# Optimization experiments

Hardware: AMD Instinct MI355X
Metric: run time of the kernel (lower is better)

Reference implementation:

```python
import jax, jax.numpy as jnp
import numpy as np

N = 50000   # nodes
R = 50      # relations
B = 30      # bases
F_IN = 64   # input features
H = 64      # hidden channels
C = 8       # classes
E = 1000000 # edges


def setup_inputs() -> dict:
    key = jax.random.key(0)
    ks = jax.random.split(key, 16)
    x = jax.random.normal(ks[0], (N, F_IN), jnp.float32)
    edge_index = jax.random.randint(ks[1], (2, E), 0, N)
    edge_type = jax.random.randint(ks[2], (E,), 0, R)
    inp = {"x": x, "edge_index": edge_index, "edge_type": edge_type}
    dims = [(F_IN, H), (H, H), (H, C)]
    i = 3
    for l, (din, dout) in enumerate(dims):
        s = 1.0 / np.sqrt(din)
        inp[f"bases{l}"] = jax.random.normal(ks[i], (B, din, dout), jnp.float32) * s; i += 1
        inp[f"comp{l}"] = jax.random.normal(ks[i], (R, B), jnp.float32) / np.sqrt(B); i += 1
        inp[f"root{l}"] = jax.random.normal(ks[i], (din, dout), jnp.float32) * s; i += 1
        inp[f"bias{l}"] = jnp.zeros((dout,), jnp.float32); i += 1
    return inp


def _rgcn(x, bases, comp, root, bias, src, seg):
    # Per-relation mean aggregation (PyG RGCNConv default aggr='mean'):
    # segment id = dst * R + relation. Mean of source features per (dst, rel),
    # then basis-decomposed transform (linearity lets transform follow the mean).
    din = x.shape[1]
    sums = jax.ops.segment_sum(x[src], seg, num_segments=N * R)          # [N*R, din]
    cnt = jax.ops.segment_sum(jnp.ones((seg.shape[0],), x.dtype), seg, num_segments=N * R)
    inv = jnp.where(cnt > 0, 1.0 / jnp.maximum(cnt, 1.0), 0.0)
    agg = (sums * inv[:, None]).reshape(N, R, din)                        # [N, R, din]
    t = jnp.einsum('nri,rb->nbi', agg, comp)                              # [N, B, din]
    msg = jnp.einsum('nbi,bio->no', t, bases)                             # [N, dout]
    return msg + x @ root + bias


def reference(x, edge_index, edge_type,
              bases0, comp0, root0, bias0,
              bases1, comp1, root1, bias1,
              bases2, comp2, root2, bias2):
    src, dst = edge_index[0], edge_index[1]
    seg = dst * R + edge_type
    params = [(bases0, comp0, root0, bias0),
              (bases1, comp1, root1, bias1),
              (bases2, comp2, root2, bias2)]
    x1 = x
    for b, c, r, bi in params:
        x1 = _rgcn(x, b, c, r, bi, src, seg)
        x = jax.nn.relu(x1)
    # original returns log_softmax of the last conv's pre-ReLU output
    return jax.nn.log_softmax(x1, axis=1)
```

## Files before the change

kernel.cpp:

```cpp
#include <hip/hip_runtime.h>
#include <hip/hip_bf16.h>
#include <stdint.h>

#define NN   50000
#define RR   50
#define BB   30
#define DIN  64
#define EE   1000000
#define KTOT (BB*DIN + DIN)
#define NBW  16
#define ROWE (KTOT + 8)
#define CPAD 32

typedef __attribute__((ext_vector_type(8))) short short8;
typedef __attribute__((ext_vector_type(4))) float floatx4;

#define RFL(x) __builtin_amdgcn_readfirstlane(x)


__global__ void k_hist(const int* __restrict__ dst, const int* __restrict__ et,
                       int* __restrict__ cnt, int* __restrict__ dcount) {
    int e = blockIdx.x * 256 + threadIdx.x;
    if (e < EE) {
        int d = dst[e], r = et[e];
        atomicAdd(&cnt[d * RR + r], 1);
        atomicAdd(&dcount[d], 1);
    }
}

__global__ void k_scan1(const int* __restrict__ dcount, int* __restrict__ doff,
                        int* __restrict__ bsum) {
    __shared__ int sh[256];
    int t = threadIdx.x;
    int i = blockIdx.x * 256 + t;
    int v = (i < NN) ? dcount[i] : 0;
    sh[t] = v;
    __syncthreads();
    for (int s = 1; s < 256; s <<= 1) {
        int add = (t >= s) ? sh[t - s] : 0;
        __syncthreads();
        sh[t] += add;
        __syncthreads();
    }
    int incl = sh[t];
    if (i < NN) doff[i] = incl - v;
    if (t == 255) bsum[blockIdx.x] = incl;
}

__global__ void k_scan2(int* __restrict__ bsum, int nbv) {
    __shared__ int sh[256];
    int t = threadIdx.x;
    int v = (t < nbv) ? bsum[t] : 0;
    sh[t] = v;
    __syncthreads();
    for (int s = 1; s < 256; s <<= 1) {
        int add = (t >= s) ? sh[t - s] : 0;
        __syncthreads();
        sh[t] += add;
        __syncthreads();
    }
    if (t < nbv) bsum[t] = sh[t] - v;
}

__global__ void k_scan3(int* __restrict__ doff, const int* __restrict__ bsum) {
    int i = blockIdx.x * 256 + threadIdx.x;
    if (i < NN) doff[i] += bsum[blockIdx.x];
}

__global__ void k_scatter(const int* __restrict__ src, const int* __restrict__ dst,
                          const int* __restrict__ et, const int* __restrict__ cnt,
                          const int* __restrict__ doff, int* __restrict__ cursor,
                          int4* __restrict__ epack) {
    int e = blockIdx.x * 256 + threadIdx.x;
    if (e < EE) {
        int d = dst[e], r = et[e], s = src[e];
        int p = doff[d] + atomicAdd(&cursor[d], 1);
        float a = 1.0f / (float)cnt[d * RR + r];
        epack[p] = make_int4(s, r, __float_as_int(a), 0);
    }
}

__global__ void k_cast_x(const float* __restrict__ x, __hip_bfloat16* __restrict__ h) {
    int i = blockIdx.x * 256 + threadIdx.x;
    if (i < NN * DIN) h[i] = __float2bfloat16(x[i]);
}

__global__ void k_prep_comp3(const float* __restrict__ c0, const float* __restrict__ c1,
                             const float* __restrict__ c2, float* __restrict__ cp) {
    int idx = blockIdx.x * 256 + threadIdx.x;
    if (idx < 3 * RR * CPAD) {
        int l = idx / (RR * CPAD);
        int rem = idx - l * (RR * CPAD);
        int r = rem / CPAD, i = rem - r * CPAD;
        const float* c = (l == 0) ? c0 : (l == 1) ? c1 : c2;
        cp[idx] = (i < BB) ? c[r * BB + i] : 0.f;
    }
}

__global__ void k_prep_w3(const float* __restrict__ b0, const float* __restrict__ r0,
                          const float* __restrict__ b1, const float* __restrict__ r1,
                          const float* __restrict__ b2, const float* __restrict__ r2,
                          short* __restrict__ wt) {
    int idx = blockIdx.x * 256 + threadIdx.x;
    if (idx >= 144 * KTOT) return;
    int row = idx / KTOT, k = idx - row * KTOT;
    const float* bs; const float* rt; int o, dout;
    if (row < 64)       { bs = b0; rt = r0; o = row;        dout = 64; }
    else if (row < 128) { bs = b1; rt = r1; o = row - 64;   dout = 64; }
    else                { bs = b2; rt = r2; o = row - 128;  dout = 8;  }
    float v = 0.f;
    if (o < dout)
        v = (k < BB * DIN) ? bs[k * dout + o] : rt[(k - BB * DIN) * dout + o];
    __hip_bfloat16 hb = __float2bfloat16(v);
    wt[idx] = *reinterpret_cast<const short*>(&hb);
}

template <int DOUT, bool RELU>
__global__ __launch_bounds__(1024, 8)
void k_fused(const __hip_bfloat16* __restrict__ xin,
             const int4* __restrict__ epack,
             const int* __restrict__ doff, const int* __restrict__ dcount,
             const float* __restrict__ compP,
             const short* __restrict__ Wt,
             const float* __restrict__ bias,
             void* __restrict__ outp) {
    __shared__ __align__(16) char smem_raw[NBW * ROWE * 2];
    auto t_tile = reinterpret_cast<__hip_bfloat16(*)[ROWE]>(smem_raw);
    const int tid  = threadIdx.x;
    const int lane = tid & 63;
    const int wv   = RFL(tid >> 6);
    const int node0 = blockIdx.x * NBW;

    {
        const int j = wv;
        const int n = node0 + j;
        floatx4 acc[8];
#pragma unroll
        for (int u = 0; u < 8; ++u) acc[u] = (floatx4){0.f, 0.f, 0.f, 0.f};
        const int beg = RFL(doff[n]), cnt = RFL(dcount[n]);
        const int nch = cnt >> 2;

        if (nch > 0) {
            int4 cr0 = epack[beg + 0], cr1 = epack[beg + 1];
            int4 cr2 = epack[beg + 2], cr3 = epack[beg + 3];
            float g0 = __bfloat162float(xin[RFL(cr0.x) * DIN + lane]);
            float g1 = __bfloat162float(xin[RFL(cr1.x) * DIN + lane]);
            float g2 = __bfloat162float(xin[RFL(cr2.x) * DIN + lane]);
            float g3 = __bfloat162float(xin[RFL(cr3.x) * DIN + lane]);
            const int b1 = beg + ((1 < nch) ? 4 : 0);
            int4 nr0 = epack[b1 + 0], nr1 = epack[b1 + 1];
            int4 nr2 = epack[b1 + 2], nr3 = epack[b1 + 3];

            for (int c = 0; c < nch; ++c) {
                const int cc = (c + 2 < nch) ? (c + 2) : (nch - 1);
                const int bp = beg + 4 * cc;
                int4 p0 = epack[bp + 0], p1 = epack[bp + 1];
                int4 p2 = epack[bp + 2], p3 = epack[bp + 3];
                float h0 = __bfloat162float(xin[RFL(nr0.x) * DIN + lane]);
                float h1 = __bfloat162float(xin[RFL(nr1.x) * DIN + lane]);
                float h2 = __bfloat162float(xin[RFL(nr2.x) * DIN + lane]);
                float h3 = __bfloat162float(xin[RFL(nr3.x) * DIN + lane]);
                {
                    const float a0 = __int_as_float(RFL(cr0.z));
                    const floatx4* q0 = (const floatx4*)(compP + RFL(cr0.y) * CPAD);
                    const float xv0 = g0 * a0;
                    const floatx4 w0 = {xv0, xv0, xv0, xv0};
#pragma unroll
                    for (int u = 0; u < 8; ++u) acc[u] = q0[u] * w0 + acc[u];
                    const float a1 = __int_as_float(RFL(cr1.z));
                    const floatx4* q1 = (const floatx4*)(compP + RFL(cr1.y) * CPAD);
                    const float xv1 = g1 * a1;
                    const floatx4 w1 = {xv1, xv1, xv1, xv1};
#pragma unroll
                    for (int u = 0; u < 8; ++u) acc[u] = q1[u] * w1 + acc[u];
                    const float a2 = __int_as_float(RFL(cr2.z));
                    const floatx4* q2 = (const floatx4*)(compP + RFL(cr2.y) * CPAD);
                    const float xv2 = g2 * a2;
                    const floatx4 w2 = {xv2, xv2, xv2, xv2};
#pragma unroll
                    for (int u = 0; u < 8; ++u) acc[u] = q2[u] * w2 + acc[u];
                    const float a3 = __int_as_float(RFL(cr3.z));
                    const floatx4* q3 = (const floatx4*)(compP + RFL(cr3.y) * CPAD);
                    const float xv3 = g3 * a3;
                    const floatx4 w3 = {xv3, xv3, xv3, xv3};
#pragma unroll
                    for (int u = 0; u < 8; ++u) acc[u] = q3[u] * w3 + acc[u];
                }
                cr0 = nr0; cr1 = nr1; cr2 = nr2; cr3 = nr3;
                nr0 = p0;  nr1 = p1;  nr2 = p2;  nr3 = p3;
                g0 = h0; g1 = h1; g2 = h2; g3 = h3;
            }
        }
        for (int e = nch * 4; e < cnt; ++e) {
            int4 ep = epack[beg + e];
            const int s = RFL(ep.x), r = RFL(ep.y);
            const float a = __int_as_float(RFL(ep.z));
            const float xv = __bfloat162float(xin[s * DIN + lane]) * a;
            const floatx4* c = (const floatx4*)(compP + r * CPAD);
            const floatx4 w = {xv, xv, xv, xv};
#pragma unroll
            for (int u = 0; u < 8; ++u) acc[u] = c[u] * w + acc[u];
        }
        const float xself = __bfloat162float(xin[n * DIN + lane]);
#pragma unroll
        for (int b = 0; b < BB; ++b)
            t_tile[j][b * DIN + lane] = __float2bfloat16(acc[b >> 2][b & 3]);
        t_tile[j][BB * DIN + lane] = __float2bfloat16(xself);
    }
    __syncthreads();

    const int m = lane & 15;
    const int q = lane >> 4;
    int kk0, nsteps, col_base, kpart;
    if (DOUT == 64) {
        kpart = wv >> 2;
        col_base = (wv & 3) * 16;
        kk0    = (kpart <= 1) ? kpart * 16 : (kpart == 2 ? 32 : 47);
        nsteps = (kpart <= 1) ? 16 : 15;
    } else {
        kpart = wv;
        col_base = 0;
        kk0    = (kpart < 14) ? kpart * 4 : (kpart == 14 ? 56 : 59);
        nsteps = (kpart < 14) ? 4 : 3;
    }
    const __hip_bfloat16* arow = &t_tile[m][q * 8];
    const short* brow = Wt + (size_t)(col_base + m) * KTOT + q * 8;

    floatx4 acc0 = {0.f, 0.f, 0.f, 0.f};
    floatx4 acc1 = {0.f, 0.f, 0.f, 0.f};
    int s = 0;
    for (; s + 2 <= nsteps; s += 2) {
        const int kk = kk0 + s;
        short8 a0 = *reinterpret_cast<const short8*>(arow + kk * 32);
        short8 b0 = *reinterpret_cast<const short8*>(brow + kk * 32);
        short8 a1 = *reinterpret_cast<const short8*>(arow + (kk + 1) * 32);
        short8 b1 = *reinterpret_cast<const short8*>(brow + (kk + 1) * 32);
        acc0 = __builtin_amdgcn_mfma_f32_16x16x32_bf16(a0, b0, acc0, 0, 0, 0);
        acc1 = __builtin_amdgcn_mfma_f32_16x16x32_bf16(a1, b1, acc1, 0, 0, 0);
    }
    if (s < nsteps) {
        const int kk = kk0 + s;
        short8 a0 = *reinterpret_cast<const short8*>(arow + kk * 32);
        short8 b0 = *reinterpret_cast<const short8*>(brow + kk * 32);
        acc0 = __builtin_amdgcn_mfma_f32_16x16x32_bf16(a0, b0, acc0, 0, 0, 0);
    }
    floatx4 P = acc0 + acc1;

    __syncthreads();
    float* red = (float*)smem_raw;

    if (DOUT == 64) {
        if (kpart > 0) {
            const int slot = (wv & 3) * 3 + (kpart - 1);
            const int off = (slot * 64 + lane) * 6;
            red[off] = P[0]; red[off + 1] = P[1]; red[off + 2] = P[2]; red[off + 3] = P[3];
        }
        __syncthreads();
        if (kpart == 0) {
#pragma unroll
            for (int t = 0; t < 3; ++t) {
                const int off = (((wv & 3) * 3 + t) * 64 + lane) * 6;
                P[0] += red[off]; P[1] += red[off + 1];
                P[2] += red[off + 2]; P[3] += red[off + 3];
            }
            const int o = col_base + m;
            const float bi = bias[o];
#pragma unroll
            for (int r = 0; r < 4; ++r) {
                const int n = node0 + q * 4 + r;
                float v = P[r] + bi;
                if (RELU) {
                    v = fmaxf(v, 0.f);
                    reinterpret_cast<__hip_bfloat16*>(outp)[(size_t)n * DOUT + o] =
                        __float2bfloat16(v);
                } else {
                    reinterpret_cast<float*>(outp)[(size_t)n * DOUT + o] = v;
                }
            }
        }
    } else {
        if (kpart > 0) {
            const int off = ((kpart - 1) * 64 + lane) * 6;
            red[off] = P[0]; red[off + 1] = P[1]; red[off + 2] = P[2]; red[off + 3] = P[3];
        }
        __syncthreads();
        if (kpart == 0) {
#pragma unroll
            for (int w = 0; w < 15; ++w) {
                const int off = (w * 64 + lane) * 6;
                P[0] += red[off]; P[1] += red[off + 1];
                P[2] += red[off + 2]; P[3] += red[off + 3];
            }
            if (m < DOUT) {
                const int o = m;
                const float bi = bias[o];
#pragma unroll
                for (int r = 0; r < 4; ++r) {
                    const int n = node0 + q * 4 + r;
                    reinterpret_cast<float*>(outp)[(size_t)n * DOUT + o] = P[r] + bi;
                }
            }
        }
    }
}

__global__ void k_lsm(const float* __restrict__ pre, float* __restrict__ out) {
    int n = blockIdx.x * 256 + threadIdx.x;
    if (n < NN) {
        float v[8];
        float mx = -1e30f;
#pragma unroll
        for (int c = 0; c < 8; ++c) { v[c] = pre[n * 8 + c]; mx = fmaxf(mx, v[c]); }
        float s = 0.f;
#pragma unroll
        for (int c = 0; c < 8; ++c) s += expf(v[c] - mx);
        float ls = logf(s);
#pragma unroll
        for (int c = 0; c < 8; ++c) out[n * 8 + c] = v[c] - mx - ls;
    }
}

extern "C" void kernel_launch(void* const* d_in, const int* in_sizes, int n_in,
                              void* d_out, int out_size, void* d_ws, size_t ws_size,
                              hipStream_t stream) {
    const float* x     = (const float*)d_in[0];
    const int*   eidx  = (const int*)d_in[1];
    const int*   etype = (const int*)d_in[2];
    const float* bases0 = (const float*)d_in[3];
    const float* comp0  = (const float*)d_in[4];
    const float* root0  = (const float*)d_in[5];
    const float* bias0  = (const float*)d_in[6];
    const float* bases1 = (const float*)d_in[7];
    const float* comp1  = (const float*)d_in[8];
    const float* root1  = (const float*)d_in[9];
    const float* bias1  = (const float*)d_in[10];
    const float* bases2 = (const float*)d_in[11];
    const float* comp2  = (const float*)d_in[12];
    const float* root2  = (const float*)d_in[13];
    const float* bias2  = (const float*)d_in[14];
    const int* srcp = eidx;
    const int* dstp = eidx + EE;

    char* p = (char*)d_ws;
    auto carve = [&](size_t bytes) -> char* {
        char* r = p;
        p += (bytes + 255) & ~(size_t)255;
        return r;
    };
    int*  cnt    = (int*)carve((size_t)NN * RR * sizeof(int));
    int*  dcount = (int*)carve((size_t)NN * sizeof(int));
    int*  cursor = (int*)carve((size_t)NN * sizeof(int));
    int*  doff   = (int*)carve((size_t)NN * sizeof(int));
    int*  bsum   = (int*)carve(256 * sizeof(int));
    int4* epack  = (int4*)carve((size_t)EE * sizeof(int4));
    __hip_bfloat16* h0 = (__hip_bfloat16*)carve((size_t)NN * DIN * 2);
    __hip_bfloat16* h1 = (__hip_bfloat16*)carve((size_t)NN * DIN * 2);
    __hip_bfloat16* h2 = (__hip_bfloat16*)carve((size_t)NN * DIN * 2);
    float* pre = (float*)carve((size_t)NN * 8 * sizeof(float));
    short* wtA = (short*)carve((size_t)144 * KTOT * sizeof(short));
    float* cpA = (float*)carve((size_t)3 * RR * CPAD * sizeof(float));

    hipMemsetAsync(cnt, 0, (size_t)NN * (RR + 2) * sizeof(int) + 512, stream);

    const int EB = (EE + 255) / 256;
    const int NB = (NN + 255) / 256;
    k_hist<<<EB, 256, 0, stream>>>(dstp, etype, cnt, dcount);
    k_scan1<<<NB, 256, 0, stream>>>(dcount, doff, bsum);
    k_scan2<<<1, 256, 0, stream>>>(bsum, NB);
    k_scan3<<<NB, 256, 0, stream>>>(doff, bsum);
    k_scatter<<<EB, 256, 0, stream>>>(srcp, dstp, etype, cnt, doff, cursor, epack);
    k_cast_x<<<(NN * DIN + 255) / 256, 256, 0, stream>>>(x, h0);
    k_prep_comp3<<<(3 * RR * CPAD + 255) / 256, 256, 0, stream>>>(comp0, comp1, comp2, cpA);
    k_prep_w3<<<(144 * KTOT + 255) / 256, 256, 0, stream>>>(bases0, root0, bases1, root1,
                                                            bases2, root2, wtA);

    short* wt0 = wtA;
    short* wt1 = wtA + (size_t)64 * KTOT;
    short* wt2 = wtA + (size_t)128 * KTOT;
    float* cp0 = cpA;
    float* cp1 = cpA + RR * CPAD;
    float* cp2 = cpA + 2 * RR * CPAD;

    const int NF = NN / NBW;
    k_fused<64, true ><<<NF, 1024, 0, stream>>>(h0, epack, doff, dcount, cp0, wt0, bias0, (void*)h1);
    k_fused<64, true ><<<NF, 1024, 0, stream>>>(h1, epack, doff, dcount, cp1, wt1, bias1, (void*)h2);
    k_fused<8,  false><<<NF, 1024, 0, stream>>>(h2, epack, doff, dcount, cp2, wt2, bias2, (void*)pre);
    k_lsm<<<NB, 256, 0, stream>>>(pre, (float*)d_out);
}
```

Before: 598.5 us.

## Process two nodes per wave with packed 8-byte edge records and 512-thread blocks

The fused RGCN kernel now uses 512-thread blocks, and each wave aggregates two destination nodes in one software-pipelined loop. Partial 4-edge chunks are padded with zeroed records, which removes the scalar tail loop. Edge records shrink from int4 to int2 by packing source and relation into one word, halving edge-stream traffic. The per-destination degree atomic is dropped and degrees are recomputed in the scan from the per-relation counts. The GEMM K-split is rebalanced for 8 waves. The packing assumes node ids below 65536 and uses fewer waves per block, which may reduce latency hiding.

```diff
diff --git a/kernel.cpp b/kernel.cpp
--- a/kernel.cpp
+++ b/kernel.cpp
@@ -19,21 +19,26 @@
 
 
 __global__ void k_hist(const int* __restrict__ dst, const int* __restrict__ et,
-                       int* __restrict__ cnt, int* __restrict__ dcount) {
+                       int* __restrict__ cnt) {
     int e = blockIdx.x * 256 + threadIdx.x;
     if (e < EE) {
         int d = dst[e], r = et[e];
         atomicAdd(&cnt[d * RR + r], 1);
-        atomicAdd(&dcount[d], 1);
-    }
-}
-
-__global__ void k_scan1(const int* __restrict__ dcount, int* __restrict__ doff,
-                        int* __restrict__ bsum) {
+    }
+}
+
+__global__ void k_scan1(const int* __restrict__ cnt, int* __restrict__ dcount,
+                        int* __restrict__ doff, int* __restrict__ bsum) {
     __shared__ int sh[256];
     int t = threadIdx.x;
     int i = blockIdx.x * 256 + t;
-    int v = (i < NN) ? dcount[i] : 0;
+    int v = 0;
+    if (i < NN) {
+        const int* c = cnt + (size_t)i * RR;
+#pragma unroll
+        for (int r = 0; r < RR; ++r) v += c[r];
+        dcount[i] = v;
+    }
     sh[t] = v;
     __syncthreads();
     for (int s = 1; s < 256; s <<= 1) {
@@ -70,13 +75,13 @@
 __global__ void k_scatter(const int* __restrict__ src, const int* __restrict__ dst,
                           const int* __restrict__ et, const int* __restrict__ cnt,
                           const int* __restrict__ doff, int* __restrict__ cursor,
-                          int4* __restrict__ epack) {
+                          int2* __restrict__ ep2) {
     int e = blockIdx.x * 256 + threadIdx.x;
     if (e < EE) {
         int d = dst[e], r = et[e], s = src[e];
         int p = doff[d] + atomicAdd(&cursor[d], 1);
         float a = 1.0f / (float)cnt[d * RR + r];
-        epack[p] = make_int4(s, r, __float_as_int(a), 0);
+        ep2[p] = make_int2(s | (r << 16), __float_as_int(a));
     }
 }
 
@@ -115,10 +120,37 @@
     wt[idx] = *reinterpret_cast<const short*>(&hb);
 }
 
+
+#define LOADREC(u, q0, q1, q2, q3) do {                                         \
+    const int _u  = (u);                                                        \
+    const int _b  = (_u < nchA) ? (begA + 4*_u) : (begB + 4*(_u - nchA));       \
+    const int _rm = (_u < nchA) ? (cntA - 4*_u) : (cntB - 4*(_u - nchA));       \
+    q0 = ep2[_b];     q1 = ep2[_b + 1];                                         \
+    q2 = ep2[_b + 2]; q3 = ep2[_b + 3];                                         \
+    q1.x = (_rm > 1) ? q1.x : 0;  q1.y = (_rm > 1) ? q1.y : 0;                  \
+    q2.x = (_rm > 2) ? q2.x : 0;  q2.y = (_rm > 2) ? q2.y : 0;                  \
+    q3.x = (_rm > 3) ? q3.x : 0;  q3.y = (_rm > 3) ? q3.y : 0;                  \
+} while (0)
+
+#define GATH(q) ((unsigned)xin16[(RFL((q).x) & 0xFFFF) * DIN + lane])
+
+#define EDGE_FMA(q, g, ACC) do {                                                \
+    const int   _sx = RFL((q).x);                                               \
+    const float _a  = __int_as_float(RFL((q).y));                               \
+    const floatx4* _c = (const floatx4*)(compP + (_sx >> 16) * CPAD);           \
+    const float _g  = __uint_as_float((g) << 16);              \
+    const float _xv = _g * _a;                                                  \
+    const floatx4 _w = {_xv, _xv, _xv, _xv};                                    \
+    ACC[0] = _c[0] * _w + ACC[0];  ACC[1] = _c[1] * _w + ACC[1];                \
+    ACC[2] = _c[2] * _w + ACC[2];  ACC[3] = _c[3] * _w + ACC[3];                \
+    ACC[4] = _c[4] * _w + ACC[4];  ACC[5] = _c[5] * _w + ACC[5];                \
+    ACC[6] = _c[6] * _w + ACC[6];  ACC[7] = _c[7] * _w + ACC[7];                \
+} while (0)
+
 template <int DOUT, bool RELU>
-__global__ __launch_bounds__(1024, 8)
+__global__ __launch_bounds__(512, 4)
 void k_fused(const __hip_bfloat16* __restrict__ xin,
-             const int4* __restrict__ epack,
+             const int2* __restrict__ ep2,
              const int* __restrict__ doff, const int* __restrict__ dcount,
              const float* __restrict__ compP,
              const short* __restrict__ Wt,
@@ -126,86 +158,63 @@
              void* __restrict__ outp) {
     __shared__ __align__(16) char smem_raw[NBW * ROWE * 2];
     auto t_tile = reinterpret_cast<__hip_bfloat16(*)[ROWE]>(smem_raw);
+    const unsigned short* xin16 = reinterpret_cast<const unsigned short*>(xin);
     const int tid  = threadIdx.x;
     const int lane = tid & 63;
     const int wv   = RFL(tid >> 6);
     const int node0 = blockIdx.x * NBW;
+    const int nA = node0 + wv;
+    const int nB = node0 + wv + 8;
 
     {
-        const int j = wv;
-        const int n = node0 + j;
-        floatx4 acc[8];
-#pragma unroll
-        for (int u = 0; u < 8; ++u) acc[u] = (floatx4){0.f, 0.f, 0.f, 0.f};
-        const int beg = RFL(doff[n]), cnt = RFL(dcount[n]);
-        const int nch = cnt >> 2;
-
-        if (nch > 0) {
-            int4 cr0 = epack[beg + 0], cr1 = epack[beg + 1];
-            int4 cr2 = epack[beg + 2], cr3 = epack[beg + 3];
-            float g0 = __bfloat162float(xin[RFL(cr0.x) * DIN + lane]);
-            float g1 = __bfloat162float(xin[RFL(cr1.x) * DIN + lane]);
-            float g2 = __bfloat162float(xin[RFL(cr2.x) * DIN + lane]);
-            float g3 = __bfloat162float(xin[RFL(cr3.x) * DIN + lane]);
-            const int b1 = beg + ((1 < nch) ? 4 : 0);
-            int4 nr0 = epack[b1 + 0], nr1 = epack[b1 + 1];
-            int4 nr2 = epack[b1 + 2], nr3 = epack[b1 + 3];
-
-            for (int c = 0; c < nch; ++c) {
-                const int cc = (c + 2 < nch) ? (c + 2) : (nch - 1);
-                const int bp = beg + 4 * cc;
-                int4 p0 = epack[bp + 0], p1 = epack[bp + 1];
-                int4 p2 = epack[bp + 2], p3 = epack[bp + 3];
-                float h0 = __bfloat162float(xin[RFL(nr0.x) * DIN + lane]);
-                float h1 = __bfloat162float(xin[RFL(nr1.x) * DIN + lane]);
-                float h2 = __bfloat162float(xin[RFL(nr2.x) * DIN + lane]);
-                float h3 = __bfloat162float(xin[RFL(nr3.x) * DIN + lane]);
-                {
-                    const float a0 = __int_as_float(RFL(cr0.z));
-                    const floatx4* q0 = (const floatx4*)(compP + RFL(cr0.y) * CPAD);
-                    const float xv0 = g0 * a0;
-                    const floatx4 w0 = {xv0, xv0, xv0, xv0};
-#pragma unroll
-                    for (int u = 0; u < 8; ++u) acc[u] = q0[u] * w0 + acc[u];
-                    const float a1 = __int_as_float(RFL(cr1.z));
-                    const floatx4* q1 = (const floatx4*)(compP + RFL(cr1.y) * CPAD);
-                    const float xv1 = g1 * a1;
-                    const floatx4 w1 = {xv1, xv1, xv1, xv1};
-#pragma unroll
-                    for (int u = 0; u < 8; ++u) acc[u] = q1[u] * w1 + acc[u];
-                    const float a2 = __int_as_float(RFL(cr2.z));
-                    const floatx4* q2 = (const floatx4*)(compP + RFL(cr2.y) * CPAD);
-                    const float xv2 = g2 * a2;
-                    const floatx4 w2 = {xv2, xv2, xv2, xv2};
-#pragma unroll
-                    for (int u = 0; u < 8; ++u) acc[u] = q2[u] * w2 + acc[u];
-                    const float a3 = __int_as_float(RFL(cr3.z));
-                    const floatx4* q3 = (const floatx4*)(compP + RFL(cr3.y) * CPAD);
-                    const float xv3 = g3 * a3;
-                    const floatx4 w3 = {xv3, xv3, xv3, xv3};
-#pragma unroll
-                    for (int u = 0; u < 8; ++u) acc[u] = q3[u] * w3 + acc[u];
+        floatx4 accA[8], accB[8];
+#pragma unroll
+        for (int u = 0; u < 8; ++u) {
+            accA[u] = (floatx4){0.f, 0.f, 0.f, 0.f};
+            accB[u] = (floatx4){0.f, 0.f, 0.f, 0.f};
+        }
+        const unsigned selfA = (unsigned)xin16[nA * DIN + lane];
+        const unsigned selfB = (unsigned)xin16[nB * DIN + lane];
+
+        const int begA = RFL(doff[nA]), cntA = RFL(dcount[nA]);
+        const int begB = RFL(doff[nB]), cntB = RFL(dcount[nB]);
+        const int nchA = (cntA + 3) >> 2;
+        const int nchB = (cntB + 3) >> 2;
+        const int T = nchA + nchB;
+
+        if (T > 0) {
+            int2 c0, c1, c2, c3, n0, n1, n2, n3;
+            LOADREC(0, c0, c1, c2, c3);
+            unsigned g0 = GATH(c0), g1 = GATH(c1), g2 = GATH(c2), g3 = GATH(c3);
+            { const int u1 = (1 < T) ? 1 : 0; LOADREC(u1, n0, n1, n2, n3); }
+
+            for (int t = 0; t < T; ++t) {
+                int2 p0, p1, p2, p3;
+                { const int u2 = (t + 2 < T) ? (t + 2) : (T - 1);
+                  LOADREC(u2, p0, p1, p2, p3); }
+                unsigned h0 = GATH(n0), h1 = GATH(n1), h2 = GATH(n2), h3 = GATH(n3);
+                if (t < nchA) {
+                    EDGE_FMA(c0, g0, accA); EDGE_FMA(c1, g1, accA);
+                    EDGE_FMA(c2, g2, accA); EDGE_FMA(c3, g3, accA);
+                } else {
+                    EDGE_FMA(c0, g0, accB); EDGE_FMA(c1, g1, accB);
+                    EDGE_FMA(c2, g2, accB); EDGE_FMA(c3, g3, accB);
                 }
-                cr0 = nr0; cr1 = nr1; cr2 = nr2; cr3 = nr3;
-                nr0 = p0;  nr1 = p1;  nr2 = p2;  nr3 = p3;
+                c0 = n0; c1 = n1; c2 = n2; c3 = n3;
+                n0 = p0; n1 = p1; n2 = p2; n3 = p3;
                 g0 = h0; g1 = h1; g2 = h2; g3 = h3;
             }
         }
-        for (int e = nch * 4; e < cnt; ++e) {
-            int4 ep = epack[beg + e];
-            const int s = RFL(ep.x), r = RFL(ep.y);
-            const float a = __int_as_float(RFL(ep.z));
-            const float xv = __bfloat162float(xin[s * DIN + lane]) * a;
-            const floatx4* c = (const floatx4*)(compP + r * CPAD);
-            const floatx4 w = {xv, xv, xv, xv};
-#pragma unroll
-            for (int u = 0; u < 8; ++u) acc[u] = c[u] * w + acc[u];
-        }
-        const float xself = __bfloat162float(xin[n * DIN + lane]);
 #pragma unroll
         for (int b = 0; b < BB; ++b)
-            t_tile[j][b * DIN + lane] = __float2bfloat16(acc[b >> 2][b & 3]);
-        t_tile[j][BB * DIN + lane] = __float2bfloat16(xself);
+            t_tile[wv][b * DIN + lane] = __float2bfloat16(accA[b >> 2][b & 3]);
+        t_tile[wv][BB * DIN + lane] =
+            __float2bfloat16(__uint_as_float(selfA << 16));
+#pragma unroll
+        for (int b = 0; b < BB; ++b)
+            t_tile[wv + 8][b * DIN + lane] = __float2bfloat16(accB[b >> 2][b & 3]);
+        t_tile[wv + 8][BB * DIN + lane] =
+            __float2bfloat16(__uint_as_float(selfB << 16));
     }
     __syncthreads();
 
@@ -215,13 +224,13 @@
     if (DOUT == 64) {
         kpart = wv >> 2;
         col_base = (wv & 3) * 16;
-        kk0    = (kpart <= 1) ? kpart * 16 : (kpart == 2 ? 32 : 47);
-        nsteps = (kpart <= 1) ? 16 : 15;
+        kk0    = kpart * 31;
+        nsteps = 31;
     } else {
         kpart = wv;
         col_base = 0;
-        kk0    = (kpart < 14) ? kpart * 4 : (kpart == 14 ? 56 : 59);
-        nsteps = (kpart < 14) ? 4 : 3;
+        kk0    = (kpart < 7) ? kpart * 8 : 55;
+        nsteps = (kpart < 6) ? 8 : 7;
     }
     const __hip_bfloat16* arow = &t_tile[m][q * 8];
     const short* brow = Wt + (size_t)(col_base + m) * KTOT + q * 8;
@@ -250,19 +259,15 @@
     float* red = (float*)smem_raw;
 
     if (DOUT == 64) {
-        if (kpart > 0) {
-            const int slot = (wv & 3) * 3 + (kpart - 1);
-            const int off = (slot * 64 + lane) * 6;
+        if (kpart == 1) {
+            const int off = ((wv & 3) * 64 + lane) * 6;
             red[off] = P[0]; red[off + 1] = P[1]; red[off + 2] = P[2]; red[off + 3] = P[3];
         }
         __syncthreads();
         if (kpart == 0) {
-#pragma unroll
-            for (int t = 0; t < 3; ++t) {
-                const int off = (((wv & 3) * 3 + t) * 64 + lane) * 6;
-                P[0] += red[off]; P[1] += red[off + 1];
-                P[2] += red[off + 2]; P[3] += red[off + 3];
-            }
+            const int off = ((wv & 3) * 64 + lane) * 6;
+            P[0] += red[off]; P[1] += red[off + 1];
+            P[2] += red[off + 2]; P[3] += red[off + 3];
             const int o = col_base + m;
             const float bi = bias[o];
 #pragma unroll
@@ -286,7 +291,7 @@
         __syncthreads();
         if (kpart == 0) {
 #pragma unroll
-            for (int w = 0; w < 15; ++w) {
+            for (int w = 0; w < 7; ++w) {
                 const int off = (w * 64 + lane) * 6;
                 P[0] += red[off]; P[1] += red[off + 1];
                 P[2] += red[off + 2]; P[3] += red[off + 3];
@@ -352,7 +357,7 @@
     int*  cursor = (int*)carve((size_t)NN * sizeof(int));
     int*  doff   = (int*)carve((size_t)NN * sizeof(int));
     int*  bsum   = (int*)carve(256 * sizeof(int));
-    int4* epack  = (int4*)carve((size_t)EE * sizeof(int4));
+    int2* ep2    = (int2*)carve((size_t)(EE + 8) * sizeof(int2));
     __hip_bfloat16* h0 = (__hip_bfloat16*)carve((size_t)NN * DIN * 2);
     __hip_bfloat16* h1 = (__hip_bfloat16*)carve((size_t)NN * DIN * 2);
     __hip_bfloat16* h2 = (__hip_bfloat16*)carve((size_t)NN * DIN * 2);
@@ -364,11 +369,11 @@
 
     const int EB = (EE + 255) / 256;
     const int NB = (NN + 255) / 256;
-    k_hist<<<EB, 256, 0, stream>>>(dstp, etype, cnt, dcount);
-    k_scan1<<<NB, 256, 0, stream>>>(dcount, doff, bsum);
+    k_hist<<<EB, 256, 0, stream>>>(dstp, etype, cnt);
+    k_scan1<<<NB, 256, 0, stream>>>(cnt, dcount, doff, bsum);
     k_scan2<<<1, 256, 0, stream>>>(bsum, NB);
     k_scan3<<<NB, 256, 0, stream>>>(doff, bsum);
-    k_scatter<<<EB, 256, 0, stream>>>(srcp, dstp, etype, cnt, doff, cursor, epack);
+    k_scatter<<<EB, 256, 0, stream>>>(srcp, dstp, etype, cnt, doff, cursor, ep2);
     k_cast_x<<<(NN * DIN + 255) / 256, 256, 0, stream>>>(x, h0);
     k_prep_comp3<<<(3 * RR * CPAD + 255) / 256, 256, 0, stream>>>(comp0, comp1, comp2, cpA);
     k_prep_w3<<<(144 * KTOT + 255) / 256, 256, 0, stream>>>(bases0, root0, bases1, root1,
@@ -382,8 +387,8 @@
     float* cp2 = cpA + 2 * RR * CPAD;
 
     const int NF = NN / NBW;
-    k_fused<64, true ><<<NF, 1024, 0, stream>>>(h0, epack, doff, dcount, cp0, wt0, bias0, (void*)h1);
-    k_fused<64, true ><<<NF, 1024, 0, stream>>>(h1, epack, doff, dcount, cp1, wt1, bias1, (void*)h2);
-    k_fused<8,  false><<<NF, 1024, 0, stream>>>(h2, epack, doff, dcount, cp2, wt2, bias2, (void*)pre);
+    k_fused<64, true ><<<NF, 512, 0, stream>>>(h0, ep2, doff, dcount, cp0, wt0, bias0, (void*)h1);
+    k_fused<64, true ><<<NF, 512, 0, stream>>>(h1, ep2, doff, dcount, cp1, wt1, bias1, (void*)h2);
+    k_fused<8,  false><<<NF, 512, 0, stream>>>(h2, ep2, doff, dcount, cp2, wt2, bias2, (void*)pre);
     k_lsm<<<NB, 256, 0, stream>>>(pre, (float*)d_out);
 }
```

New measurement: 720.9 us. 20.4% more time.

## Pack edges into 8 bytes, sort nodes by degree, derive degrees from histogram

Applied to the files above, without the earlier changes.

Edge records shrink from int4 to int2 by packing source index and relation into one word, halving edge-stream traffic in the three fused layers. Nodes are counting-sorted by in-degree (descending) so each 16-node block handles waves with similar edge counts, reducing load imbalance across waves. Per-node degree is now computed by summing the per-relation count row instead of a second atomic in the histogram. This adds three small preprocessing kernels and an indirection through the order array, and scatters output rows non-contiguously.

```diff
diff --git a/kernel.cpp b/kernel.cpp
--- a/kernel.cpp
+++ b/kernel.cpp
@@ -19,21 +19,26 @@
 
 
 __global__ void k_hist(const int* __restrict__ dst, const int* __restrict__ et,
-                       int* __restrict__ cnt, int* __restrict__ dcount) {
+                       int* __restrict__ cnt) {
     int e = blockIdx.x * 256 + threadIdx.x;
     if (e < EE) {
         int d = dst[e], r = et[e];
         atomicAdd(&cnt[d * RR + r], 1);
-        atomicAdd(&dcount[d], 1);
-    }
-}
-
-__global__ void k_scan1(const int* __restrict__ dcount, int* __restrict__ doff,
-                        int* __restrict__ bsum) {
+    }
+}
+
+__global__ void k_scan1(const int* __restrict__ cnt, int* __restrict__ dcount,
+                        int* __restrict__ doff, int* __restrict__ bsum) {
     __shared__ int sh[256];
     int t = threadIdx.x;
     int i = blockIdx.x * 256 + t;
-    int v = (i < NN) ? dcount[i] : 0;
+    int v = 0;
+    if (i < NN) {
+        const int* c = cnt + (size_t)i * RR;
+#pragma unroll
+        for (int r = 0; r < RR; ++r) v += c[r];
+        dcount[i] = v;
+    }
     sh[t] = v;
     __syncthreads();
     for (int s = 1; s < 256; s <<= 1) {
@@ -70,13 +75,48 @@
 __global__ void k_scatter(const int* __restrict__ src, const int* __restrict__ dst,
                           const int* __restrict__ et, const int* __restrict__ cnt,
                           const int* __restrict__ doff, int* __restrict__ cursor,
-                          int4* __restrict__ epack) {
+                          int2* __restrict__ ep2) {
     int e = blockIdx.x * 256 + threadIdx.x;
     if (e < EE) {
         int d = dst[e], r = et[e], s = src[e];
         int p = doff[d] + atomicAdd(&cursor[d], 1);
         float a = 1.0f / (float)cnt[d * RR + r];
-        epack[p] = make_int4(s, r, __float_as_int(a), 0);
+        ep2[p] = make_int2(s | (r << 16), __float_as_int(a));
+    }
+}
+
+
+__global__ void k_deghist(const int* __restrict__ dcount, int* __restrict__ dbin) {
+    int i = blockIdx.x * 256 + threadIdx.x;
+    if (i < NN) {
+        int d = dcount[i]; d = (d > 255) ? 255 : d;
+        atomicAdd(&dbin[255 - d], 1);
+    }
+}
+
+__global__ void k_degscan(int* __restrict__ dbin) {
+    __shared__ int sh[256];
+    int t = threadIdx.x;
+    int v = dbin[t];
+    sh[t] = v;
+    __syncthreads();
+    for (int s = 1; s < 256; s <<= 1) {
+        int add = (t >= s) ? sh[t - s] : 0;
+        __syncthreads();
+        sh[t] += add;
+        __syncthreads();
+    }
+    dbin[t] = sh[t] - v;
+}
+
+__global__ void k_degscatter(const int* __restrict__ dcount, const int* __restrict__ dbin,
+                             int* __restrict__ dcur, int* __restrict__ order) {
+    int i = blockIdx.x * 256 + threadIdx.x;
+    if (i < NN) {
+        int d = dcount[i]; d = (d > 255) ? 255 : d;
+        int b = 255 - d;
+        int pos = dbin[b] + atomicAdd(&dcur[b], 1);
+        order[pos] = i;
     }
 }
 
@@ -118,14 +158,16 @@
 template <int DOUT, bool RELU>
 __global__ __launch_bounds__(1024, 8)
 void k_fused(const __hip_bfloat16* __restrict__ xin,
-             const int4* __restrict__ epack,
+             const int2* __restrict__ ep2,
              const int* __restrict__ doff, const int* __restrict__ dcount,
+             const int* __restrict__ order,
              const float* __restrict__ compP,
              const short* __restrict__ Wt,
              const float* __restrict__ bias,
              void* __restrict__ outp) {
     __shared__ __align__(16) char smem_raw[NBW * ROWE * 2];
     auto t_tile = reinterpret_cast<__hip_bfloat16(*)[ROWE]>(smem_raw);
+    const unsigned short* xin16 = reinterpret_cast<const unsigned short*>(xin);
     const int tid  = threadIdx.x;
     const int lane = tid & 63;
     const int wv   = RFL(tid >> 6);
@@ -133,7 +175,7 @@
 
     {
         const int j = wv;
-        const int n = node0 + j;
+        const int n = RFL(order[node0 + j]);
         floatx4 acc[8];
 #pragma unroll
         for (int u = 0; u < 8; ++u) acc[u] = (floatx4){0.f, 0.f, 0.f, 0.f};
@@ -141,46 +183,50 @@
         const int nch = cnt >> 2;
 
         if (nch > 0) {
-            int4 cr0 = epack[beg + 0], cr1 = epack[beg + 1];
-            int4 cr2 = epack[beg + 2], cr3 = epack[beg + 3];
-            float g0 = __bfloat162float(xin[RFL(cr0.x) * DIN + lane]);
-            float g1 = __bfloat162float(xin[RFL(cr1.x) * DIN + lane]);
-            float g2 = __bfloat162float(xin[RFL(cr2.x) * DIN + lane]);
-            float g3 = __bfloat162float(xin[RFL(cr3.x) * DIN + lane]);
+            int2 cr0 = ep2[beg + 0], cr1 = ep2[beg + 1];
+            int2 cr2 = ep2[beg + 2], cr3 = ep2[beg + 3];
+            float g0 = __bfloat162float(xin[(RFL(cr0.x) & 0xFFFF) * DIN + lane]);
+            float g1 = __bfloat162float(xin[(RFL(cr1.x) & 0xFFFF) * DIN + lane]);
+            float g2 = __bfloat162float(xin[(RFL(cr2.x) & 0xFFFF) * DIN + lane]);
+            float g3 = __bfloat162float(xin[(RFL(cr3.x) & 0xFFFF) * DIN + lane]);
             const int b1 = beg + ((1 < nch) ? 4 : 0);
-            int4 nr0 = epack[b1 + 0], nr1 = epack[b1 + 1];
-            int4 nr2 = epack[b1 + 2], nr3 = epack[b1 + 3];
+            int2 nr0 = ep2[b1 + 0], nr1 = ep2[b1 + 1];
+            int2 nr2 = ep2[b1 + 2], nr3 = ep2[b1 + 3];
 
             for (int c = 0; c < nch; ++c) {
                 const int cc = (c + 2 < nch) ? (c + 2) : (nch - 1);
                 const int bp = beg + 4 * cc;
-                int4 p0 = epack[bp + 0], p1 = epack[bp + 1];
-                int4 p2 = epack[bp + 2], p3 = epack[bp + 3];
-                float h0 = __bfloat162float(xin[RFL(nr0.x) * DIN + lane]);
-                float h1 = __bfloat162float(xin[RFL(nr1.x) * DIN + lane]);
-                float h2 = __bfloat162float(xin[RFL(nr2.x) * DIN + lane]);
-                float h3 = __bfloat162float(xin[RFL(nr3.x) * DIN + lane]);
+                int2 p0 = ep2[bp + 0], p1 = ep2[bp + 1];
+                int2 p2 = ep2[bp + 2], p3 = ep2[bp + 3];
+                float h0 = __bfloat162float(xin[(RFL(nr0.x) & 0xFFFF) * DIN + lane]);
+                float h1 = __bfloat162float(xin[(RFL(nr1.x) & 0xFFFF) * DIN + lane]);
+                float h2 = __bfloat162float(xin[(RFL(nr2.x) & 0xFFFF) * DIN + lane]);
+                float h3 = __bfloat162float(xin[(RFL(nr3.x) & 0xFFFF) * DIN + lane]);
                 {
-                    const float a0 = __int_as_float(RFL(cr0.z));
-                    const floatx4* q0 = (const floatx4*)(compP + RFL(cr0.y) * CPAD);
+                    const int sx0 = RFL(cr0.x);
+                    const float a0 = __int_as_float(RFL(cr0.y));
+                    const floatx4* q0 = (const floatx4*)(compP + (sx0 >> 16) * CPAD);
                     const float xv0 = g0 * a0;
                     const floatx4 w0 = {xv0, xv0, xv0, xv0};
 #pragma unroll
                     for (int u = 0; u < 8; ++u) acc[u] = q0[u] * w0 + acc[u];
-                    const float a1 = __int_as_float(RFL(cr1.z));
-                    const floatx4* q1 = (const floatx4*)(compP + RFL(cr1.y) * CPAD);
+                    const int sx1 = RFL(cr1.x);
+                    const float a1 = __int_as_float(RFL(cr1.y));
+                    const floatx4* q1 = (const floatx4*)(compP + (sx1 >> 16) * CPAD);
                     const float xv1 = g1 * a1;
                     const floatx4 w1 = {xv1, xv1, xv1, xv1};
 #pragma unroll
                     for (int u = 0; u < 8; ++u) acc[u] = q1[u] * w1 + acc[u];
-                    const float a2 = __int_as_float(RFL(cr2.z));
-                    const floatx4* q2 = (const floatx4*)(compP + RFL(cr2.y) * CPAD);
+                    const int sx2 = RFL(cr2.x);
+                    const float a2 = __int_as_float(RFL(cr2.y));
+                    const floatx4* q2 = (const floatx4*)(compP + (sx2 >> 16) * CPAD);
                     const float xv2 = g2 * a2;
                     const floatx4 w2 = {xv2, xv2, xv2, xv2};
 #pragma unroll
                     for (int u = 0; u < 8; ++u) acc[u] = q2[u] * w2 + acc[u];
-                    const float a3 = __int_as_float(RFL(cr3.z));
-                    const floatx4* q3 = (const floatx4*)(compP + RFL(cr3.y) * CPAD);
+                    const int sx3 = RFL(cr3.x);
+                    const float a3 = __int_as_float(RFL(cr3.y));
+                    const floatx4* q3 = (const floatx4*)(compP + (sx3 >> 16) * CPAD);
                     const float xv3 = g3 * a3;
                     const floatx4 w3 = {xv3, xv3, xv3, xv3};
 #pragma unroll
@@ -192,11 +238,11 @@
             }
         }
         for (int e = nch * 4; e < cnt; ++e) {
-            int4 ep = epack[beg + e];
-            const int s = RFL(ep.x), r = RFL(ep.y);
-            const float a = __int_as_float(RFL(ep.z));
-            const float xv = __bfloat162float(xin[s * DIN + lane]) * a;
-            const floatx4* c = (const floatx4*)(compP + r * CPAD);
+            int2 ep = ep2[beg + e];
+            const int sx = RFL(ep.x);
+            const float a = __int_as_float(RFL(ep.y));
+            const float xv = __bfloat162float(xin[(sx & 0xFFFF) * DIN + lane]) * a;
+            const floatx4* c = (const floatx4*)(compP + (sx >> 16) * CPAD);
             const floatx4 w = {xv, xv, xv, xv};
 #pragma unroll
             for (int u = 0; u < 8; ++u) acc[u] = c[u] * w + acc[u];
@@ -267,7 +313,7 @@
             const float bi = bias[o];
 #pragma unroll
             for (int r = 0; r < 4; ++r) {
-                const int n = node0 + q * 4 + r;
+                const int n = order[node0 + q * 4 + r];
                 float v = P[r] + bi;
                 if (RELU) {
                     v = fmaxf(v, 0.f);
@@ -296,7 +342,7 @@
                 const float bi = bias[o];
 #pragma unroll
                 for (int r = 0; r < 4; ++r) {
-                    const int n = node0 + q * 4 + r;
+                    const int n = order[node0 + q * 4 + r];
                     reinterpret_cast<float*>(outp)[(size_t)n * DOUT + o] = P[r] + bi;
                 }
             }
@@ -352,7 +398,10 @@
     int*  cursor = (int*)carve((size_t)NN * sizeof(int));
     int*  doff   = (int*)carve((size_t)NN * sizeof(int));
     int*  bsum   = (int*)carve(256 * sizeof(int));
-    int4* epack  = (int4*)carve((size_t)EE * sizeof(int4));
+    int*  dbin   = (int*)carve(256 * sizeof(int));
+    int*  dcur   = (int*)carve(256 * sizeof(int));
+    int*  order  = (int*)carve((size_t)NN * sizeof(int));
+    int2* ep2    = (int2*)carve((size_t)(EE + 8) * sizeof(int2));
     __hip_bfloat16* h0 = (__hip_bfloat16*)carve((size_t)NN * DIN * 2);
     __hip_bfloat16* h1 = (__hip_bfloat16*)carve((size_t)NN * DIN * 2);
     __hip_bfloat16* h2 = (__hip_bfloat16*)carve((size_t)NN * DIN * 2);
@@ -361,14 +410,18 @@
     float* cpA = (float*)carve((size_t)3 * RR * CPAD * sizeof(float));
 
     hipMemsetAsync(cnt, 0, (size_t)NN * (RR + 2) * sizeof(int) + 512, stream);
+    hipMemsetAsync(dbin, 0, 2048, stream);
 
     const int EB = (EE + 255) / 256;
     const int NB = (NN + 255) / 256;
-    k_hist<<<EB, 256, 0, stream>>>(dstp, etype, cnt, dcount);
-    k_scan1<<<NB, 256, 0, stream>>>(dcount, doff, bsum);
+    k_hist<<<EB, 256, 0, stream>>>(dstp, etype, cnt);
+    k_scan1<<<NB, 256, 0, stream>>>(cnt, dcount, doff, bsum);
     k_scan2<<<1, 256, 0, stream>>>(bsum, NB);
     k_scan3<<<NB, 256, 0, stream>>>(doff, bsum);
-    k_scatter<<<EB, 256, 0, stream>>>(srcp, dstp, etype, cnt, doff, cursor, epack);
+    k_scatter<<<EB, 256, 0, stream>>>(srcp, dstp, etype, cnt, doff, cursor, ep2);
+    k_deghist<<<NB, 256, 0, stream>>>(dcount, dbin);
+    k_degscan<<<1, 256, 0, stream>>>(dbin);
+    k_degscatter<<<NB, 256, 0, stream>>>(dcount, dbin, dcur, order);
     k_cast_x<<<(NN * DIN + 255) / 256, 256, 0, stream>>>(x, h0);
     k_prep_comp3<<<(3 * RR * CPAD + 255) / 256, 256, 0, stream>>>(comp0, comp1, comp2, cpA);
     k_prep_w3<<<(144 * KTOT + 255) / 256, 256, 0, stream>>>(bases0, root0, bases1, root1,
@@ -382,8 +435,8 @@
     float* cp2 = cpA + 2 * RR * CPAD;
 
     const int NF = NN / NBW;
-    k_fused<64, true ><<<NF, 1024, 0, stream>>>(h0, epack, doff, dcount, cp0, wt0, bias0, (void*)h1);
-    k_fused<64, true ><<<NF, 1024, 0, stream>>>(h1, epack, doff, dcount, cp1, wt1, bias1, (void*)h2);
-    k_fused<8,  false><<<NF, 1024, 0, stream>>>(h2, epack, doff, dcount, cp2, wt2, bias2, (void*)pre);
+    k_fused<64, true ><<<NF, 1024, 0, stream>>>(h0, ep2, doff, dcount, order, cp0, wt0, bias0, (void*)h1);
+    k_fused<64, true ><<<NF, 1024, 0, stream>>>(h1, ep2, doff, dcount, order, cp1, wt1, bias1, (void*)h2);
+    k_fused<8,  false><<<NF, 1024, 0, stream>>>(h2, ep2, doff, dcount, order, cp2, wt2, bias2, (void*)pre);
     k_lsm<<<NB, 256, 0, stream>>>(pre, (float*)d_out);
 }
```

Result: slower. 829.3 us (+38.6%).
